# Performance work log

Hardware: AMD Instinct MI355X
Metric: run time of the kernel (lower is better)

The kernel has to match this reference:

```python
import jax, jax.numpy as jnp
import numpy as np

N_NODES = 50000
N_EDGES = 1600000
IN_DIM = 1024
HID = 2048
OUT = 3
BN_EPS = 1e-5


def _degree_norms(src, dst):
    ones = jnp.ones((src.shape[0],), jnp.float32)
    out_deg = jax.ops.segment_sum(ones, src, num_segments=N_NODES)
    in_deg = jax.ops.segment_sum(ones, dst, num_segments=N_NODES)
    # DGL GraphConv norm='both' clamps degrees to min 1
    out_norm = jnp.clip(out_deg, 1.0) ** -0.5
    in_norm = jnp.clip(in_deg, 1.0) ** -0.5
    return out_norm, in_norm


def _graph_conv(h, src, dst, out_norm, in_norm, W, b):
    # symmetric-normalized SpMM aggregate then dense transform (DGL GraphConv, norm='both')
    h = h * out_norm[:, None]
    msg = h[src]                                   # [E, F] gather
    agg = jax.ops.segment_sum(msg, dst, num_segments=N_NODES)
    agg = agg * in_norm[:, None]
    return agg @ W + b


def setup_inputs() -> dict:
    key = jax.random.key(0)
    k1, k2, k3, k4, k5, k6, k7 = jax.random.split(key, 7)
    in_feat = jax.random.normal(k1, (N_NODES, IN_DIM), jnp.float32)
    src = jax.random.randint(k2, (N_EDGES,), 0, N_NODES, jnp.int32)
    dst = jax.random.randint(k3, (N_EDGES,), 0, N_NODES, jnp.int32)
    W1 = jax.random.normal(k4, (IN_DIM, HID), jnp.float32) * (1.0 / np.sqrt(IN_DIM))
    b1 = jnp.zeros((HID,), jnp.float32)
    Wout = jax.random.normal(k5, (HID, OUT), jnp.float32) * (1.0 / np.sqrt(HID))
    bout = jnp.zeros((OUT,), jnp.float32)
    return {"in_feat": in_feat, "src": src, "dst": dst,
            "W1": W1, "b1": b1, "Wout": Wout, "bout": bout}


def reference(in_feat, src, dst, W1, b1, Wout, bout):
    out_norm, in_norm = _degree_norms(src, dst)
    h = _graph_conv(in_feat, src, dst, out_norm, in_norm, W1, b1)
    h = jax.nn.relu(h)
    # freshly-instantiated BatchNorm1d in training mode: batch stats, gamma=1, beta=0
    mean = jnp.mean(h, axis=0, keepdims=True)
    var = jnp.var(h, axis=0, keepdims=True)
    h = (h - mean) * jax.lax.rsqrt(var + BN_EPS)
    h = _graph_conv(h, src, dst, out_norm, in_norm, Wout, bout)
    return jax.nn.softmax(h, axis=1)
```

## Files before the change

kernel.cpp:

```cpp
#include <hip/hip_runtime.h>
#include <hip/hip_bf16.h>
#include <stdint.h>

#define N_NODES 50000
#define N_EDGES 1600000
#define IN_DIM  1024
#define HID     2048
#define OUTC    3
#define M_PAD   50048
#define BN_EPS  1e-5f

#define SCAN_CH 512
#define NCH     98

#define NPANEL  2
#define PFEAT   512

typedef __bf16 bf16_t;
typedef __bf16 bf16x4_t __attribute__((ext_vector_type(4)));
typedef __bf16 bf16x8_t __attribute__((ext_vector_type(8)));
typedef float  f32x4_t  __attribute__((ext_vector_type(4)));

__device__ __forceinline__ void gl2lds16(const void* g, void* l) {
  __builtin_amdgcn_global_load_lds((const __attribute__((address_space(1))) uint32_t*)g,
                                   (__attribute__((address_space(3))) uint32_t*)l,
                                   16, 0, 0);
}

__global__ void k_hist(const int* __restrict__ src, const int* __restrict__ dst,
                       int* out_cnt, int* in_cnt) {
  int e = blockIdx.x * 256 + threadIdx.x;
  if (e < N_EDGES) {
    atomicAdd(&out_cnt[src[e]], 1);
    atomicAdd(&in_cnt[dst[e]], 1);
  }
}

__global__ void k_norms(const int* __restrict__ out_cnt, const int* __restrict__ in_cnt,
                        float* out_norm, float* in_norm) {
  int i = blockIdx.x * 256 + threadIdx.x;
  if (i < N_NODES) {
    out_norm[i] = rsqrtf((float)max(out_cnt[i], 1));
    in_norm[i]  = rsqrtf((float)max(in_cnt[i], 1));
  }
}

__global__ void k_scan1(const int* __restrict__ deg, int* incl, int* partial) {
  __shared__ int s[SCAN_CH];
  int tid = threadIdx.x;
  int i = blockIdx.x * SCAN_CH + tid;
  int v = (i < N_NODES) ? deg[i] : 0;
  s[tid] = v;
  for (int off = 1; off < SCAN_CH; off <<= 1) {
    __syncthreads();
    int x = (tid >= off) ? s[tid - off] : 0;
    __syncthreads();
    s[tid] += x;
  }
  __syncthreads();
  if (i < N_NODES) incl[i] = s[tid];
  if (tid == SCAN_CH - 1) partial[blockIdx.x] = s[tid];
}

__global__ void k_scan2(const int* __restrict__ partial, int* chunk_off, int* row_ptr) {
  if (threadIdx.x == 0 && blockIdx.x == 0) {
    int run = 0;
    for (int b = 0; b < NCH; b++) { chunk_off[b] = run; run += partial[b]; }
    row_ptr[N_NODES] = run;
  }
}

__global__ void k_scan3(const int* __restrict__ deg, const int* __restrict__ incl,
                        const int* __restrict__ chunk_off, int* row_ptr, int* cursor) {
  int i = blockIdx.x * SCAN_CH + threadIdx.x;
  if (i < N_NODES) {
    int e = chunk_off[blockIdx.x] + incl[i] - deg[i];
    row_ptr[i] = e;
    cursor[i]  = e;
  }
}

__global__ void k_fill(const int* __restrict__ src, const int* __restrict__ dst,
                       int* cursor, int* csr_src) {
  int e = blockIdx.x * 256 + threadIdx.x;
  if (e < N_EDGES) {
    int p = atomicAdd(&cursor[dst[e]], 1);
    csr_src[p] = src[e];
  }
}

__global__ void k_conv(const float* __restrict__ in_feat, const float* __restrict__ out_norm,
                       bf16_t* __restrict__ xb) {
  int node = blockIdx.x, tid = threadIdx.x;
  float on = out_norm[node];
  float4 v = *(const float4*)(in_feat + (size_t)node * IN_DIM + tid * 4);
  bf16x4_t o;
  o[0] = (bf16_t)(v.x * on); o[1] = (bf16_t)(v.y * on);
  o[2] = (bf16_t)(v.z * on); o[3] = (bf16_t)(v.w * on);
  *(bf16x4_t*)(xb + (size_t)node * IN_DIM + tid * 4) = o;
}

__global__ void k_agg1(const bf16_t* __restrict__ xb, const int* __restrict__ row_ptr,
                       const int* __restrict__ csr_src, const float* __restrict__ in_norm,
                       bf16_t* __restrict__ aggb) {
  int node = blockIdx.x * 2 + (threadIdx.x >> 6);
  int lane = threadIdx.x & 63;
  int f0 = blockIdx.y * PFEAT + lane * 8;
  float acc[8];
#pragma unroll
  for (int j = 0; j < 8; j++) acc[j] = 0.f;
  float inn = 0.f;
  if (node < N_NODES) {
    int beg = row_ptr[node], end = row_ptr[node + 1];
    int e = beg;
    for (; e + 8 <= end; e += 8) {
      int s[8];
#pragma unroll
      for (int u = 0; u < 8; u++) s[u] = csr_src[e + u];
      bf16x8_t v[8];
#pragma unroll
      for (int u = 0; u < 8; u++)
        v[u] = *(const bf16x8_t*)(xb + (size_t)s[u] * IN_DIM + f0);
#pragma unroll
      for (int u = 0; u < 8; u++)
#pragma unroll
        for (int j = 0; j < 8; j++) acc[j] += (float)v[u][j];
    }
    for (; e + 2 <= end; e += 2) {
      int s0 = csr_src[e], s1 = csr_src[e + 1];
      bf16x8_t v0 = *(const bf16x8_t*)(xb + (size_t)s0 * IN_DIM + f0);
      bf16x8_t v1 = *(const bf16x8_t*)(xb + (size_t)s1 * IN_DIM + f0);
#pragma unroll
      for (int j = 0; j < 8; j++) acc[j] += (float)v0[j];
#pragma unroll
      for (int j = 0; j < 8; j++) acc[j] += (float)v1[j];
    }
    if (e < end) {
      int s0 = csr_src[e];
      bf16x8_t v0 = *(const bf16x8_t*)(xb + (size_t)s0 * IN_DIM + f0);
#pragma unroll
      for (int j = 0; j < 8; j++) acc[j] += (float)v0[j];
    }
    inn = in_norm[node];
  }
  bf16x8_t o;
#pragma unroll
  for (int j = 0; j < 8; j++) o[j] = (bf16_t)(acc[j] * inn);
  __builtin_nontemporal_store(o, (bf16x8_t*)(aggb + (size_t)node * IN_DIM + f0));
}

__global__ void k_w1t(const float* __restrict__ W1, bf16_t* __restrict__ W1t) {
  __shared__ float tile[32][33];
  int k0 = blockIdx.x * 32, n0 = blockIdx.y * 32;
  int tx = threadIdx.x & 31, ty = threadIdx.x >> 5;
#pragma unroll
  for (int r = 0; r < 32; r += 8)
    tile[ty + r][tx] = W1[(size_t)(k0 + ty + r) * HID + n0 + tx];
  __syncthreads();
#pragma unroll
  for (int r = 0; r < 32; r += 8)
    W1t[(size_t)(n0 + ty + r) * IN_DIM + k0 + tx] = (bf16_t)tile[tx][ty + r];
}

__global__ void __launch_bounds__(256)
k_gemm1(const bf16_t* __restrict__ A, const bf16_t* __restrict__ Bt,
        const float* __restrict__ b1, bf16_t* __restrict__ C,
        float* __restrict__ colsum, float* __restrict__ colsq) {
  __shared__ bf16_t As[128 * 32];
  __shared__ bf16_t Bs[128 * 32];
  int t = threadIdx.x;
  const int m0 = blockIdx.y * 128, n0 = blockIdx.x * 128;

  int lrow = t >> 2, lseg = t & 3;
  const bf16_t* aG0 = A + (size_t)(m0 + lrow) * IN_DIM + lseg * 8;
  const bf16_t* aG1 = aG0 + (size_t)64 * IN_DIM;
  const bf16_t* bG0 = Bt + (size_t)(n0 + lrow) * IN_DIM + lseg * 8;
  const bf16_t* bG1 = bG0 + (size_t)64 * IN_DIM;
  bf16_t* aL0 = As + t * 8; bf16_t* aL1 = As + 2048 + t * 8;
  bf16_t* bL0 = Bs + t * 8; bf16_t* bL1 = Bs + 2048 + t * 8;

  int wv = t >> 6, ln = t & 63;
  int wm = (wv >> 1) * 64, wn = (wv & 1) * 64;
  int fr = ln & 15, fq = ln >> 4;
  const bf16_t* aF = As + (wm + fr) * 32 + fq * 8;
  const bf16_t* bF = Bs + (wn + fr) * 32 + fq * 8;

  f32x4_t acc[4][4];
#pragma unroll
  for (int i = 0; i < 4; i++)
#pragma unroll
    for (int j = 0; j < 4; j++) { acc[i][j][0]=0.f; acc[i][j][1]=0.f; acc[i][j][2]=0.f; acc[i][j][3]=0.f; }

  for (int kt = 0; kt < IN_DIM; kt += 32) {
    __syncthreads();
    gl2lds16(aG0 + kt, aL0);
    gl2lds16(aG1 + kt, aL1);
    gl2lds16(bG0 + kt, bL0);
    gl2lds16(bG1 + kt, bL1);
    __syncthreads();
    bf16x8_t af[4], bfr[4];
#pragma unroll
    for (int i = 0; i < 4; i++) af[i]  = *(const bf16x8_t*)(aF + i * 16 * 32);
#pragma unroll
    for (int j = 0; j < 4; j++) bfr[j] = *(const bf16x8_t*)(bF + j * 16 * 32);
#pragma unroll
    for (int i = 0; i < 4; i++)
#pragma unroll
      for (int j = 0; j < 4; j++)
        acc[i][j] = __builtin_amdgcn_mfma_f32_16x16x32_bf16(af[i], bfr[j], acc[i][j], 0, 0, 0);
  }

#pragma unroll
  for (int j = 0; j < 4; j++) {
    int col = n0 + wn + j * 16 + fr;
    float bias = b1[col];
    float s = 0.f, ss = 0.f;
#pragma unroll
    for (int i = 0; i < 4; i++) {
#pragma unroll
      for (int r = 0; r < 4; r++) {
        int row = m0 + wm + i * 16 + fq * 4 + r;
        float v = acc[i][j][r] + bias;
        v = v > 0.f ? v : 0.f;
        bf16_t bv = (bf16_t)v;
        __builtin_nontemporal_store(*(short*)&bv, (short*)&C[(size_t)row * HID + col]);
        if (row < N_NODES) { s += v; ss += v * v; }
      }
    }
    s  += __shfl_xor(s, 16);  s  += __shfl_xor(s, 32);
    ss += __shfl_xor(ss, 16); ss += __shfl_xor(ss, 32);
    if (fq == 0) {
      atomicAdd(&colsum[col], s);
      atomicAdd(&colsq[col], ss);
    }
  }
}

__global__ void k_bnfin(const float* __restrict__ colsum, const float* __restrict__ colsq,
                        const float* __restrict__ Wout,
                        float* cw0, float* cw1, float* cw2, float* mrs) {
  int f = blockIdx.x * 256 + threadIdx.x;
  if (f < HID) {
    float mean = colsum[f] * (1.f / N_NODES);
    float var  = colsq[f] * (1.f / N_NODES) - mean * mean;
    float rs   = rsqrtf(var + BN_EPS);
    cw0[f] = rs * Wout[f * 3 + 0];
    cw1[f] = rs * Wout[f * 3 + 1];
    cw2[f] = rs * Wout[f * 3 + 2];
    mrs[f] = mean * rs;
  }
}

__global__ void k_ct(const float* __restrict__ mrs, const float* __restrict__ Wout, float* ct) {
  __shared__ float red[3][256];
  int tid = threadIdx.x;
  float s0 = 0.f, s1 = 0.f, s2 = 0.f;
  for (int f = tid; f < HID; f += 256) {
    float m = mrs[f];
    s0 += m * Wout[f * 3 + 0];
    s1 += m * Wout[f * 3 + 1];
    s2 += m * Wout[f * 3 + 2];
  }
  red[0][tid] = s0; red[1][tid] = s1; red[2][tid] = s2;
  __syncthreads();
  for (int off = 128; off; off >>= 1) {
    if (tid < off) {
      red[0][tid] += red[0][tid + off];
      red[1][tid] += red[1][tid + off];
      red[2][tid] += red[2][tid + off];
    }
    __syncthreads();
  }
  if (tid == 0) { ct[0] = red[0][0]; ct[1] = red[1][0]; ct[2] = red[2][0]; }
}

__global__ void k_tmat(const bf16_t* __restrict__ h1, const float* __restrict__ cw0,
                       const float* __restrict__ cw1, const float* __restrict__ cw2,
                       const float* __restrict__ ct, const float* __restrict__ out_norm,
                       float4* __restrict__ t4) {
  int n = blockIdx.x, tid = threadIdx.x;
  int f0 = tid * 8;
  bf16x8_t hv = *(const bf16x8_t*)(h1 + (size_t)n * HID + f0);
  float s0 = 0.f, s1 = 0.f, s2 = 0.f;
#pragma unroll
  for (int j = 0; j < 8; j++) {
    float h = (float)hv[j];
    s0 += h * cw0[f0 + j];
    s1 += h * cw1[f0 + j];
    s2 += h * cw2[f0 + j];
  }
#pragma unroll
  for (int off = 32; off; off >>= 1) {
    s0 += __shfl_down(s0, off);
    s1 += __shfl_down(s1, off);
    s2 += __shfl_down(s2, off);
  }
  __shared__ float red[3][4];
  int wv = tid >> 6, ln = tid & 63;
  if (ln == 0) { red[0][wv] = s0; red[1][wv] = s1; red[2][wv] = s2; }
  __syncthreads();
  if (tid == 0) {
    float r0 = red[0][0] + red[0][1] + red[0][2] + red[0][3];
    float r1 = red[1][0] + red[1][1] + red[1][2] + red[1][3];
    float r2 = red[2][0] + red[2][1] + red[2][2] + red[2][3];
    float on = out_norm[n];
    t4[n] = make_float4(on * (r0 - ct[0]), on * (r1 - ct[1]), on * (r2 - ct[2]), 0.f);
  }
}

__global__ void k_out(const int* __restrict__ row_ptr, const int* __restrict__ csr_src,
                      const float4* __restrict__ t4, const float* __restrict__ in_norm,
                      const float* __restrict__ bout, float* __restrict__ out) {
  int i = blockIdx.x * 256 + threadIdx.x;
  if (i >= N_NODES) return;
  float a0 = 0.f, a1 = 0.f, a2 = 0.f;
  int beg = row_ptr[i], end = row_ptr[i + 1];
  for (int e = beg; e < end; e++) {
    float4 tv = t4[csr_src[e]];
    a0 += tv.x; a1 += tv.y; a2 += tv.z;
  }
  float inn = in_norm[i];
  float l0 = inn * a0 + bout[0];
  float l1 = inn * a1 + bout[1];
  float l2 = inn * a2 + bout[2];
  float m = fmaxf(l0, fmaxf(l1, l2));
  float e0 = expf(l0 - m), e1 = expf(l1 - m), e2 = expf(l2 - m);
  float rs = 1.f / (e0 + e1 + e2);
  out[i * 3 + 0] = e0 * rs;
  out[i * 3 + 1] = e1 * rs;
  out[i * 3 + 2] = e2 * rs;
}

extern "C" void kernel_launch(void* const* d_in, const int* in_sizes, int n_in,
                              void* d_out, int out_size, void* d_ws, size_t ws_size,
                              hipStream_t stream) {
  const float* in_feat = (const float*)d_in[0];
  const int*   src     = (const int*)d_in[1];
  const int*   dst     = (const int*)d_in[2];
  const float* W1      = (const float*)d_in[3];
  const float* b1      = (const float*)d_in[4];
  const float* Wout    = (const float*)d_in[5];
  const float* bout    = (const float*)d_in[6];
  float* out = (float*)d_out;

  char* p = (char*)d_ws;
  auto alloc = [&](size_t bytes) { char* r = p; p += (bytes + 255) & ~(size_t)255; return r; };
  bf16_t* h1      = (bf16_t*)alloc((size_t)M_PAD * HID * 2);
  bf16_t* aggb    = (bf16_t*)alloc((size_t)M_PAD * IN_DIM * 2);
  bf16_t* xb      = (bf16_t*)alloc((size_t)N_NODES * IN_DIM * 2);
  bf16_t* W1t     = (bf16_t*)alloc((size_t)HID * IN_DIM * 2);
  int* csr_src    = (int*)alloc((size_t)N_EDGES * 4);
  int* row_ptr    = (int*)alloc((size_t)(N_NODES + 1) * 4);
  int* cursor     = (int*)alloc((size_t)N_NODES * 4);
  int* incl       = (int*)alloc((size_t)N_NODES * 4);
  int* partial    = (int*)alloc((size_t)NCH * 4);
  int* chunk_off  = (int*)alloc((size_t)NCH * 4);
  int* out_cnt    = (int*)alloc((size_t)N_NODES * 4);
  int* in_cnt     = (int*)alloc((size_t)N_NODES * 4);
  float* out_norm = (float*)alloc((size_t)N_NODES * 4);
  float* in_norm  = (float*)alloc((size_t)N_NODES * 4);
  float* colsum   = (float*)alloc((size_t)HID * 4);
  float* colsq    = (float*)alloc((size_t)HID * 4);
  float* cw0      = (float*)alloc((size_t)HID * 4);
  float* cw1      = (float*)alloc((size_t)HID * 4);
  float* cw2      = (float*)alloc((size_t)HID * 4);
  float* mrs      = (float*)alloc((size_t)HID * 4);
  float* ct       = (float*)alloc(4 * 4);
  float4* t4      = (float4*)alloc((size_t)N_NODES * 16);

  hipMemsetAsync(out_cnt, 0, (size_t)N_NODES * 4, stream);
  hipMemsetAsync(in_cnt,  0, (size_t)N_NODES * 4, stream);
  hipMemsetAsync(colsum,  0, (size_t)HID * 4, stream);
  hipMemsetAsync(colsq,   0, (size_t)HID * 4, stream);

  k_hist <<<(N_EDGES + 255) / 256, 256, 0, stream>>>(src, dst, out_cnt, in_cnt);
  k_norms<<<(N_NODES + 255) / 256, 256, 0, stream>>>(out_cnt, in_cnt, out_norm, in_norm);
  k_conv <<<N_NODES, 256, 0, stream>>>(in_feat, out_norm, xb);
  k_scan1<<<NCH, SCAN_CH, 0, stream>>>(in_cnt, incl, partial);
  k_scan2<<<1, 64, 0, stream>>>(partial, chunk_off, row_ptr);
  k_scan3<<<NCH, SCAN_CH, 0, stream>>>(in_cnt, incl, chunk_off, row_ptr, cursor);
  k_fill <<<(N_EDGES + 255) / 256, 256, 0, stream>>>(src, dst, cursor, csr_src);
  k_w1t  <<<dim3(IN_DIM / 32, HID / 32), 256, 0, stream>>>(W1, W1t);
  k_agg1 <<<dim3(M_PAD / 2, NPANEL), 128, 0, stream>>>(xb, row_ptr, csr_src, in_norm, aggb);
  k_gemm1<<<dim3(HID / 128, M_PAD / 128), 256, 0, stream>>>(aggb, W1t, b1, h1, colsum, colsq);
  k_bnfin<<<HID / 256, 256, 0, stream>>>(colsum, colsq, Wout, cw0, cw1, cw2, mrs);
  k_ct   <<<1, 256, 0, stream>>>(mrs, Wout, ct);
  k_tmat <<<N_NODES, 256, 0, stream>>>(h1, cw0, cw1, cw2, ct, out_norm, t4);
  k_out  <<<(N_NODES + 255) / 256, 256, 0, stream>>>(row_ptr, csr_src, t4, in_norm, bout, out);
}
```

Measured before the change: 1.446 ms.

## Remap GEMM blocks for XCD locality, persist tmat, fuse scan offset pass

The GEMM grid becomes a 1D launch whose block index is decoded so that consecutive blocks on the same XCD share row tiles. This is meant to improve L2 reuse of A and B panels on the multi-die GPU. k_tmat becomes a persistent kernel with 512 blocks that stage the three weight vectors in LDS once and then loop over nodes, cutting redundant global loads and block launch overhead. The serial k_scan2 launch is folded into k_scan3 through an in-block scan of the chunk partials, which removes one kernel launch. In exchange, some GEMM blocks exit early, and k_tmat adds an extra barrier per node.

```diff
diff --git a/kernel.cpp b/kernel.cpp
--- a/kernel.cpp
+++ b/kernel.cpp
@@ -8,6 +8,7 @@
 #define HID     2048
 #define OUTC    3
 #define M_PAD   50048
+#define MTILES  391
 #define BN_EPS  1e-5f
 
 #define SCAN_CH 512
@@ -62,22 +63,27 @@
   if (tid == SCAN_CH - 1) partial[blockIdx.x] = s[tid];
 }
 
-__global__ void k_scan2(const int* __restrict__ partial, int* chunk_off, int* row_ptr) {
-  if (threadIdx.x == 0 && blockIdx.x == 0) {
-    int run = 0;
-    for (int b = 0; b < NCH; b++) { chunk_off[b] = run; run += partial[b]; }
-    row_ptr[N_NODES] = run;
-  }
-}
-
 __global__ void k_scan3(const int* __restrict__ deg, const int* __restrict__ incl,
-                        const int* __restrict__ chunk_off, int* row_ptr, int* cursor) {
-  int i = blockIdx.x * SCAN_CH + threadIdx.x;
+                        const int* __restrict__ partial, int* row_ptr, int* cursor) {
+  __shared__ int sp[128];
+  int tid = threadIdx.x;
+  if (tid < 128) sp[tid] = (tid < NCH) ? partial[tid] : 0;
+  __syncthreads();
+  for (int off = 1; off < 128; off <<= 1) {
+    int x = 0;
+    if (tid < 128 && tid >= off) x = sp[tid - off];
+    __syncthreads();
+    if (tid < 128) sp[tid] += x;
+    __syncthreads();
+  }
+  int chunk_off = (blockIdx.x == 0) ? 0 : sp[blockIdx.x - 1];
+  int i = blockIdx.x * SCAN_CH + tid;
   if (i < N_NODES) {
-    int e = chunk_off[blockIdx.x] + incl[i] - deg[i];
+    int e = chunk_off + incl[i] - deg[i];
     row_ptr[i] = e;
     cursor[i]  = e;
   }
+  if (blockIdx.x == 0 && tid == 0) row_ptr[N_NODES] = sp[NCH - 1];
 }
 
 __global__ void k_fill(const int* __restrict__ src, const int* __restrict__ dst,
@@ -168,8 +174,13 @@
         float* __restrict__ colsum, float* __restrict__ colsq) {
   __shared__ bf16_t As[128 * 32];
   __shared__ bf16_t Bs[128 * 32];
+  int bx = blockIdx.x;
+  int xcd = bx & 7, slot = bx >> 3;
+  int ct_ = slot & 15, rl = slot >> 4;
+  int r = rl * 8 + xcd;
+  if (r >= MTILES) return;
+  const int m0 = r * 128, n0 = ct_ * 128;
   int t = threadIdx.x;
-  const int m0 = blockIdx.y * 128, n0 = blockIdx.x * 128;
 
   int lrow = t >> 2, lseg = t & 3;
   const bf16_t* aG0 = A + (size_t)(m0 + lrow) * IN_DIM + lseg * 8;
@@ -218,9 +229,9 @@
 #pragma unroll
     for (int i = 0; i < 4; i++) {
 #pragma unroll
-      for (int r = 0; r < 4; r++) {
-        int row = m0 + wm + i * 16 + fq * 4 + r;
-        float v = acc[i][j][r] + bias;
+      for (int rr = 0; rr < 4; rr++) {
+        int row = m0 + wm + i * 16 + fq * 4 + rr;
+        float v = acc[i][j][rr] + bias;
         v = v > 0.f ? v : 0.f;
         bf16_t bv = (bf16_t)v;
         __builtin_nontemporal_store(*(short*)&bv, (short*)&C[(size_t)row * HID + col]);
@@ -274,37 +285,47 @@
   if (tid == 0) { ct[0] = red[0][0]; ct[1] = red[1][0]; ct[2] = red[2][0]; }
 }
 
+#define TM_BLOCKS 512
 __global__ void k_tmat(const bf16_t* __restrict__ h1, const float* __restrict__ cw0,
                        const float* __restrict__ cw1, const float* __restrict__ cw2,
                        const float* __restrict__ ct, const float* __restrict__ out_norm,
                        float4* __restrict__ t4) {
-  int n = blockIdx.x, tid = threadIdx.x;
+  __shared__ float scw0[HID], scw1[HID], scw2[HID];
+  __shared__ float red[3][4];
+  int tid = threadIdx.x;
+  for (int f = tid; f < HID; f += 256) {
+    scw0[f] = cw0[f]; scw1[f] = cw1[f]; scw2[f] = cw2[f];
+  }
+  __syncthreads();
+  float c0 = ct[0], c1 = ct[1], c2 = ct[2];
   int f0 = tid * 8;
-  bf16x8_t hv = *(const bf16x8_t*)(h1 + (size_t)n * HID + f0);
-  float s0 = 0.f, s1 = 0.f, s2 = 0.f;
-#pragma unroll
-  for (int j = 0; j < 8; j++) {
-    float h = (float)hv[j];
-    s0 += h * cw0[f0 + j];
-    s1 += h * cw1[f0 + j];
-    s2 += h * cw2[f0 + j];
-  }
-#pragma unroll
-  for (int off = 32; off; off >>= 1) {
-    s0 += __shfl_down(s0, off);
-    s1 += __shfl_down(s1, off);
-    s2 += __shfl_down(s2, off);
-  }
-  __shared__ float red[3][4];
   int wv = tid >> 6, ln = tid & 63;
-  if (ln == 0) { red[0][wv] = s0; red[1][wv] = s1; red[2][wv] = s2; }
-  __syncthreads();
-  if (tid == 0) {
-    float r0 = red[0][0] + red[0][1] + red[0][2] + red[0][3];
-    float r1 = red[1][0] + red[1][1] + red[1][2] + red[1][3];
-    float r2 = red[2][0] + red[2][1] + red[2][2] + red[2][3];
-    float on = out_norm[n];
-    t4[n] = make_float4(on * (r0 - ct[0]), on * (r1 - ct[1]), on * (r2 - ct[2]), 0.f);
+  for (int n = blockIdx.x; n < N_NODES; n += TM_BLOCKS) {
+    bf16x8_t hv = *(const bf16x8_t*)(h1 + (size_t)n * HID + f0);
+    float s0 = 0.f, s1 = 0.f, s2 = 0.f;
+#pragma unroll
+    for (int j = 0; j < 8; j++) {
+      float h = (float)hv[j];
+      s0 += h * scw0[f0 + j];
+      s1 += h * scw1[f0 + j];
+      s2 += h * scw2[f0 + j];
+    }
+#pragma unroll
+    for (int off = 32; off; off >>= 1) {
+      s0 += __shfl_down(s0, off);
+      s1 += __shfl_down(s1, off);
+      s2 += __shfl_down(s2, off);
+    }
+    if (ln == 0) { red[0][wv] = s0; red[1][wv] = s1; red[2][wv] = s2; }
+    __syncthreads();
+    if (tid == 0) {
+      float r0 = red[0][0] + red[0][1] + red[0][2] + red[0][3];
+      float r1 = red[1][0] + red[1][1] + red[1][2] + red[1][3];
+      float r2 = red[2][0] + red[2][1] + red[2][2] + red[2][3];
+      float on = out_norm[n];
+      t4[n] = make_float4(on * (r0 - c0), on * (r1 - c1), on * (r2 - c2), 0.f);
+    }
+    __syncthreads();
   }
 }
 
@@ -354,7 +375,6 @@
   int* cursor     = (int*)alloc((size_t)N_NODES * 4);
   int* incl       = (int*)alloc((size_t)N_NODES * 4);
   int* partial    = (int*)alloc((size_t)NCH * 4);
-  int* chunk_off  = (int*)alloc((size_t)NCH * 4);
   int* out_cnt    = (int*)alloc((size_t)N_NODES * 4);
   int* in_cnt     = (int*)alloc((size_t)N_NODES * 4);
   float* out_norm = (float*)alloc((size_t)N_NODES * 4);
@@ -377,14 +397,13 @@
   k_norms<<<(N_NODES + 255) / 256, 256, 0, stream>>>(out_cnt, in_cnt, out_norm, in_norm);
   k_conv <<<N_NODES, 256, 0, stream>>>(in_feat, out_norm, xb);
   k_scan1<<<NCH, SCAN_CH, 0, stream>>>(in_cnt, incl, partial);
-  k_scan2<<<1, 64, 0, stream>>>(partial, chunk_off, row_ptr);
-  k_scan3<<<NCH, SCAN_CH, 0, stream>>>(in_cnt, incl, chunk_off, row_ptr, cursor);
+  k_scan3<<<NCH, SCAN_CH, 0, stream>>>(in_cnt, incl, partial, row_ptr, cursor);
   k_fill <<<(N_EDGES + 255) / 256, 256, 0, stream>>>(src, dst, cursor, csr_src);
   k_w1t  <<<dim3(IN_DIM / 32, HID / 32), 256, 0, stream>>>(W1, W1t);
   k_agg1 <<<dim3(M_PAD / 2, NPANEL), 128, 0, stream>>>(xb, row_ptr, csr_src, in_norm, aggb);
-  k_gemm1<<<dim3(HID / 128, M_PAD / 128), 256, 0, stream>>>(aggb, W1t, b1, h1, colsum, colsq);
+  k_gemm1<<<8 * 784, 256, 0, stream>>>(aggb, W1t, b1, h1, colsum, colsq);
   k_bnfin<<<HID / 256, 256, 0, stream>>>(colsum, colsq, Wout, cw0, cw1, cw2, mrs);
   k_ct   <<<1, 256, 0, stream>>>(mrs, Wout, ct);
-  k_tmat <<<N_NODES, 256, 0, stream>>>(h1, cw0, cw1, cw2, ct, out_norm, t4);
+  k_tmat <<<TM_BLOCKS, 256, 0, stream>>>(h1, cw0, cw1, cw2, ct, out_norm, t4);
   k_out  <<<(N_NODES + 255) / 256, 256, 0, stream>>>(row_ptr, csr_src, t4, in_norm, bout, out);
 }
```

Result: slower. 1.487 ms (+2.8%).
